# Optimization experiments

Hardware: AMD Instinct MI355X
Metric: run time of the kernel (lower is better)

The kernel has to match this reference:

```python
import jax, jax.numpy as jnp
import numpy as np
import math

N, L, C, H, K = 4, 16384, 256, 8, 4
D = C // H


def setup_inputs():
    rng = jax.random.key(0)
    ks = jax.random.split(rng, 16)
    def w(k, shape, scale):
        return jax.random.normal(k, shape, jnp.float32) * scale
    s = 1.0 / math.sqrt(C)
    return {
        "query": jax.random.normal(ks[0], (N, L, C), jnp.float32),
        "key": jax.random.normal(ks[1], (N, L, C), jnp.float32),
        "value": jax.random.normal(ks[2], (N, L, C), jnp.float32),
        "reference_points": jax.random.uniform(ks[3], (N, L, 2), jnp.float32),
        "pos_embed": jax.random.normal(ks[4], (N, L, C), jnp.float32),
        "Wq": w(ks[5], (C, C), s), "bq": jnp.zeros((C,), jnp.float32),
        "Wk": w(ks[6], (C, C), s), "bk": jnp.zeros((C,), jnp.float32),
        "Wv": w(ks[7], (C, C), s), "bv": jnp.zeros((C,), jnp.float32),
        "Wo1": w(ks[8], (C, 2 * C), s), "bo1": jnp.zeros((2 * C,), jnp.float32),
        "Wo2": w(ks[9], (2 * C, H * K * 2), 0.02), "bo2": w(ks[10], (H * K * 2,), 0.02),
        "Wpos": w(ks[11], (C, C), s), "bpos": jnp.zeros((C,), jnp.float32),
        "Wout": w(ks[12], (C, C), s), "bout": jnp.zeros((C,), jnp.float32),
    }


def _sample_weight(points):
    # F.grid_sample on a 1x1 feature map (bilinear, zeros padding, align_corners=False)
    # degenerates to a scalar weight: grid g = 2p-1, unnormalized c = g/2 = p - 0.5,
    # pixel-0 bilinear weight per axis = max(0, 1 - |c|).
    c = points - 0.5
    return jax.nn.relu(1.0 - jnp.abs(c[..., 0])) * jax.nn.relu(1.0 - jnp.abs(c[..., 1]))


def reference(query, key, value, reference_points, pos_embed,
              Wq, bq, Wk, bk, Wv, bv, Wo1, bo1, Wo2, bo2, Wpos, bpos, Wout, bout):
    Nb, Ln, Cd = query.shape
    q = (query @ Wq + bq).reshape(Nb, Ln, H, D)
    k = (key @ Wk + bk).reshape(Nb, Ln, H, D)
    v = (value @ Wv + bv).reshape(Nb, Ln, H, D)
    pos = (pos_embed @ Wpos + bpos).reshape(Nb, Ln, H, D)
    q = q + pos
    k = k + pos
    # offset MLP: Linear(C,2C) -> ReLU -> Linear(2C, H*K*2)
    offsets = (jax.nn.relu(query @ Wo1 + bo1) @ Wo2 + bo2).reshape(Nb, Ln, H, K, 2)
    sp = reference_points[:, :, None, None, :] + offsets  # [N,L,H,K,2]
    w = _sample_weight(sp)                                # [N,L,H,K]
    # sampled_k[n,l,h,k,:] = k[n,l,h,:] * w[n,l,h,k]  (1x1 grid_sample closed form)
    qk = jnp.einsum('nlhd,nlhd->nlh', q, k)               # [N,L,H]
    attn = jax.nn.softmax(qk[..., None] * w / math.sqrt(D), axis=-1)  # [N,L,H,K]
    # output = sum_k attn_k * (v * w_k) = v * sum_k(attn_k * w_k)
    wv = jnp.sum(attn * w, axis=-1)                       # [N,L,H]
    out = (v * wv[..., None]).reshape(Nb, Ln, Cd)
    return out @ Wout + bout
```

## Files before the change

kernel.cpp:

```cpp
#include <hip/hip_runtime.h>
#include <hip/hip_bf16.h>

typedef __bf16 bf16x8 __attribute__((ext_vector_type(8)));
typedef float f32x4 __attribute__((ext_vector_type(4)));
typedef float f32x2 __attribute__((ext_vector_type(2)));

#define MT 32
#define CC 256

__device__ __forceinline__ int swz(int r, int c) {
    return r * 512 + ((c * 2) ^ ((r & 7) << 4));
}

template<int MREP, int NREP, int NKS>
__device__ __forceinline__ void mfma_tile(const __bf16* A_lds, const __bf16* __restrict__ WT,
                                          int KC, int ct, int kt0,
                                          f32x4 (&acc)[MREP][NREP], int r16, int q4, int laneoff)
{
#pragma unroll
    for (int ks = 0; ks < NKS; ++ks) {
        int ak = ks * 32 + q4 * 8;
        bf16x8 a[MREP], b[NREP];
#pragma unroll
        for (int mf = 0; mf < MREP; ++mf)
            a[mf] = *(const bf16x8*)((const char*)A_lds + swz(mf * 16 + r16, ak));
#pragma unroll
        for (int nf = 0; nf < NREP; ++nf)
            b[nf] = *(const bf16x8*)(WT + ((size_t)(ct + nf) * KC + kt0 + ks) * 512 + laneoff);
#pragma unroll
        for (int mf = 0; mf < MREP; ++mf)
#pragma unroll
            for (int nf = 0; nf < NREP; ++nf)
                acc[mf][nf] = __builtin_amdgcn_mfma_f32_16x16x32_bf16(a[mf], b[nf], acc[mf][nf], 0, 0, 0);
    }
}

__device__ __forceinline__ void zero4(f32x4 (&acc)[2][4]) {
#pragma unroll
    for (int i = 0; i < 2; ++i)
#pragma unroll
        for (int j = 0; j < 4; ++j)
            acc[i][j] = (f32x4){0.f, 0.f, 0.f, 0.f};
}

__device__ __forceinline__ void stage_load(const float* __restrict__ src, int row0, int tid,
                                           f32x4 (&v)[8]) {
#pragma unroll
    for (int i = 0; i < 8; ++i) {
        int f = i * 256 + tid;
        int r = f >> 6;
        int c = (f & 63) * 4;
        v[i] = __builtin_nontemporal_load((const f32x4*)(src + (size_t)(row0 + r) * CC + c));
    }
}
__device__ __forceinline__ void stage_write(__bf16* dst, int tid, const f32x4 (&v)[8]) {
#pragma unroll
    for (int i = 0; i < 8; ++i) {
        int f = i * 256 + tid;
        int r = f >> 6;
        int c = (f & 63) * 4;
        union { __bf16 h[4]; unsigned long long u; } uu;
        uu.h[0] = (__bf16)v[i][0]; uu.h[1] = (__bf16)v[i][1];
        uu.h[2] = (__bf16)v[i][2]; uu.h[3] = (__bf16)v[i][3];
        *(unsigned long long*)((char*)dst + swz(r, c)) = uu.u;
    }
}

__global__ void prep_all(const float* __restrict__ Wq, const float* __restrict__ Wk,
                         const float* __restrict__ Wpos, const float* __restrict__ Wo1,
                         const float* __restrict__ Wo2, const float* __restrict__ Wv,
                         const float* __restrict__ Wout, __bf16* __restrict__ ws)
{
    int i = blockIdx.x * 256 + threadIdx.x;
    if (i >= 557056) return;
    int j, K, N;
    const float* S0 = nullptr; const float* S1 = nullptr;
    if (i < 131072)      { j = i;          K = 512; N = 256; S0 = Wq;  S1 = Wpos; }
    else if (i < 262144) { j = i - 131072; K = 512; N = 256; S0 = Wk;  S1 = Wpos; }
    else if (i < 393216) { j = i - 262144; K = 256; N = 512; S0 = Wo1; }
    else if (i < 425984) { j = i - 393216; K = 512; N = 64;  S0 = Wo2; }
    else if (i < 491520) { j = i - 425984; K = 256; N = 256; S0 = Wv; }
    else                 { j = i - 491520; K = 256; N = 256; S0 = Wout; }
    int tile = j >> 9, r = j & 511;
    int lane = r >> 3, e = r & 7;
    int q4 = lane >> 4, r16 = lane & 15;
    int KC = K >> 5;
    int nc = tile / KC, kc = tile - nc * KC;
    int k = kc * 32 + q4 * 8 + e;
    int n = nc * 16 + r16;
    float v;
    if (S1 && k >= 256) v = S1[(size_t)(k - 256) * N + n];
    else                v = S0[(size_t)k * N + n];
    ws[i] = (__bf16)v;
}

extern "C" __global__ void __launch_bounds__(256, 2)
k1_attn_weights(const float* __restrict__ query, const float* __restrict__ key,
                const float* __restrict__ pose, const float* __restrict__ refp,
                const __bf16* __restrict__ ws,
                const float* __restrict__ bq, const float* __restrict__ bk,
                const float* __restrict__ bpos, const float* __restrict__ bo1,
                const float* __restrict__ bo2,
                float* __restrict__ wv_g)
{
    const __bf16* WTqp = ws;
    const __bf16* WTkp = ws + 131072;
    const __bf16* WTo1 = ws + 262144;
    const __bf16* WTo2 = ws + 393216;

    __shared__ __attribute__((aligned(16))) __bf16 SA[MT * CC];
    __shared__ __attribute__((aligned(16))) __bf16 SB[MT * CC];
    __shared__ __attribute__((aligned(16))) __bf16 SC[MT * CC];
    __shared__ __attribute__((aligned(16))) __bf16 SD[MT * CC];
    __shared__ float off_s[MT * 64];

    const int tid = threadIdx.x;
    const int lane = tid & 63;
    const int wid = tid >> 6;
    const int r16 = lane & 15;
    const int q4 = lane >> 4;
    const int laneoff = lane * 8;
    const int row0 = blockIdx.x * MT;
    const int cb = wid * 64;
    const int ct = wid * 4;

    f32x4 acc[2][4];
    f32x4 accO[2];

    {
        f32x4 vq[8], vp[8];
        stage_load(query, row0, tid, vq);
        stage_load(pose, row0, tid, vp);
        stage_write(SA, tid, vq);
        stage_write(SB, tid, vp);
    }
    __syncthreads();

    f32x4 vkey[8];
    stage_load(key, row0, tid, vkey);
    zero4(acc);
    mfma_tile<2, 4, 8>(SA, WTo1, 8, ct, 0, acc, r16, q4, laneoff);
#pragma unroll
    for (int mf = 0; mf < 2; ++mf)
#pragma unroll
        for (int nf = 0; nf < 4; ++nf) {
            int col = cb + nf * 16 + r16;
            float bias = bo1[col];
#pragma unroll
            for (int r = 0; r < 4; ++r)
                *(__bf16*)((char*)SD + swz(mf * 16 + q4 * 4 + r, col)) =
                    (__bf16)fmaxf(acc[mf][nf][r] + bias, 0.f);
        }
    __syncthreads();

    accO[0] = (f32x4){0.f, 0.f, 0.f, 0.f};
    accO[1] = (f32x4){0.f, 0.f, 0.f, 0.f};
    {
        f32x4 (&aO)[2][1] = *(f32x4(*)[2][1])&accO;
        mfma_tile<2, 1, 8>(SD, WTo2, 16, wid, 0, aO, r16, q4, laneoff);
    }
    __syncthreads();

    stage_write(SC, tid, vkey);
    zero4(acc);
    mfma_tile<2, 4, 8>(SA, WTo1, 8, 16 + ct, 0, acc, r16, q4, laneoff);
#pragma unroll
    for (int mf = 0; mf < 2; ++mf)
#pragma unroll
        for (int nf = 0; nf < 4; ++nf) {
            int col = cb + nf * 16 + r16;
            float bias = bo1[256 + col];
#pragma unroll
            for (int r = 0; r < 4; ++r)
                *(__bf16*)((char*)SD + swz(mf * 16 + q4 * 4 + r, col)) =
                    (__bf16)fmaxf(acc[mf][nf][r] + bias, 0.f);
        }
    __syncthreads();

    {
        f32x4 (&aO)[2][1] = *(f32x4(*)[2][1])&accO;
        mfma_tile<2, 1, 8>(SD, WTo2, 16, wid, 8, aO, r16, q4, laneoff);
    }
    {
        int col = wid * 16 + r16;
        float b2 = bo2[col];
#pragma unroll
        for (int mf = 0; mf < 2; ++mf)
#pragma unroll
            for (int r = 0; r < 4; ++r)
                off_s[(mf * 16 + q4 * 4 + r) * 64 + col] = accO[mf][r] + b2;
    }
    __syncthreads();

    zero4(acc);
    mfma_tile<2, 4, 8>(SA, WTqp, 16, ct, 0, acc, r16, q4, laneoff);
    mfma_tile<2, 4, 8>(SB, WTqp, 16, ct, 8, acc, r16, q4, laneoff);
#pragma unroll
    for (int mf = 0; mf < 2; ++mf)
#pragma unroll
        for (int nf = 0; nf < 4; ++nf) {
            int col = cb + nf * 16 + r16;
            float bias = bq[col] + bpos[col];
#pragma unroll
            for (int r = 0; r < 4; ++r)
                *(__bf16*)((char*)SD + swz(mf * 16 + q4 * 4 + r, col)) =
                    (__bf16)(acc[mf][nf][r] + bias);
        }
    __syncthreads();

    zero4(acc);
    mfma_tile<2, 4, 8>(SC, WTkp, 16, ct, 0, acc, r16, q4, laneoff);
    mfma_tile<2, 4, 8>(SB, WTkp, 16, ct, 8, acc, r16, q4, laneoff);
#pragma unroll
    for (int mf = 0; mf < 2; ++mf)
#pragma unroll
        for (int nf = 0; nf < 4; ++nf) {
            int col = cb + nf * 16 + r16;
            float bias = bk[col] + bpos[col];
#pragma unroll
            for (int r = 0; r < 4; ++r)
                *(__bf16*)((char*)SA + swz(mf * 16 + q4 * 4 + r, col)) =
                    (__bf16)(acc[mf][nf][r] + bias);
        }
    __syncthreads();

    {
        int t = tid >> 3, h = tid & 7;
        float qk = 0.f;
#pragma unroll
        for (int j = 0; j < 4; ++j) {
            int c = h * 32 + j * 8;
            bf16x8 qv = *(const bf16x8*)((const char*)SD + swz(t, c));
            bf16x8 kv = *(const bf16x8*)((const char*)SA + swz(t, c));
#pragma unroll
            for (int e = 0; e < 8; ++e) qk += (float)qv[e] * (float)kv[e];
        }
        f32x2 rp = __builtin_nontemporal_load((const f32x2*)(refp + (size_t)(row0 + t) * 2));
        float wgt[4], lg[4];
        float m = -1e30f;
#pragma unroll
        for (int kk = 0; kk < 4; ++kk) {
            float2 o = *(const float2*)&off_s[t * 64 + (h * 4 + kk) * 2];
            float cx = rp[0] + o.x - 0.5f, cy = rp[1] + o.y - 0.5f;
            float wx = fmaxf(0.f, 1.f - fabsf(cx));
            float wy = fmaxf(0.f, 1.f - fabsf(cy));
            wgt[kk] = wx * wy;
            lg[kk] = qk * wgt[kk] * 0.17677669529663687f;
            m = fmaxf(m, lg[kk]);
        }
        float s = 0.f, sw = 0.f;
#pragma unroll
        for (int kk = 0; kk < 4; ++kk) {
            float e = __expf(lg[kk] - m);
            s += e;
            sw += e * wgt[kk];
        }
        __builtin_nontemporal_store(sw / s, wv_g + (size_t)(row0 + t) * 8 + h);
    }
}

extern "C" __global__ void __launch_bounds__(256, 4)
k2_output(const float* __restrict__ value, const float* __restrict__ wv_g,
          const __bf16* __restrict__ ws,
          const float* __restrict__ bv, const float* __restrict__ bout,
          float* __restrict__ out)
{
    const __bf16* WTv   = ws + 425984;
    const __bf16* WTout = ws + 491520;

    __shared__ __attribute__((aligned(16))) __bf16 SC[MT * 256];
    __shared__ __attribute__((aligned(16))) __bf16 SD[MT * 256];
    __shared__ float wv_s[MT * 8];

    const int tid = threadIdx.x;
    const int lane = tid & 63;
    const int wid = tid >> 6;
    const int r16 = lane & 15;
    const int q4 = lane >> 4;
    const int laneoff = lane * 8;
    const int row0 = blockIdx.x * MT;
    const int cb = wid * 64;
    const int ct = wid * 4;

    f32x4 acc[2][4];

    {
        f32x4 vv[8];
        stage_load(value, row0, tid, vv);
        wv_s[tid] = wv_g[(size_t)row0 * 8 + tid];
        stage_write(SC, tid, vv);
    }
    __syncthreads();

    zero4(acc);
    mfma_tile<2, 4, 8>(SC, WTv, 8, ct, 0, acc, r16, q4, laneoff);
#pragma unroll
    for (int mf = 0; mf < 2; ++mf)
#pragma unroll
        for (int nf = 0; nf < 4; ++nf) {
            int col = cb + nf * 16 + r16;
            float bias = bv[col];
#pragma unroll
            for (int r = 0; r < 4; ++r) {
                int row = mf * 16 + q4 * 4 + r;
                float wvv = wv_s[row * 8 + (col >> 5)];
                *(__bf16*)((char*)SD + swz(row, col)) = (__bf16)((acc[mf][nf][r] + bias) * wvv);
            }
        }
    __syncthreads();

    zero4(acc);
    mfma_tile<2, 4, 8>(SD, WTout, 8, ct, 0, acc, r16, q4, laneoff);
#pragma unroll
    for (int mf = 0; mf < 2; ++mf)
#pragma unroll
        for (int nf = 0; nf < 4; ++nf) {
            int col = cb + nf * 16 + r16;
            float bias = bout[col];
#pragma unroll
            for (int r = 0; r < 4; ++r) {
                int row = mf * 16 + q4 * 4 + r;
                __builtin_nontemporal_store(acc[mf][nf][r] + bias,
                                            out + (size_t)(row0 + row) * CC + col);
            }
        }
}

extern "C" void kernel_launch(void* const* d_in, const int* in_sizes, int n_in,
                              void* d_out, int out_size, void* d_ws, size_t ws_size,
                              hipStream_t stream)
{
    const float* query = (const float*)d_in[0];
    const float* key   = (const float*)d_in[1];
    const float* value = (const float*)d_in[2];
    const float* refp  = (const float*)d_in[3];
    const float* pose  = (const float*)d_in[4];
    const float* Wq  = (const float*)d_in[5];  const float* bq   = (const float*)d_in[6];
    const float* Wk  = (const float*)d_in[7];  const float* bk   = (const float*)d_in[8];
    const float* Wv  = (const float*)d_in[9];  const float* bv   = (const float*)d_in[10];
    const float* Wo1 = (const float*)d_in[11]; const float* bo1  = (const float*)d_in[12];
    const float* Wo2 = (const float*)d_in[13]; const float* bo2  = (const float*)d_in[14];
    const float* Wpos= (const float*)d_in[15]; const float* bpos = (const float*)d_in[16];
    const float* Wout= (const float*)d_in[17]; const float* bout = (const float*)d_in[18];

    __bf16* ws = (__bf16*)d_ws;
    float* wv_g = (float*)((char*)d_ws + 1114112);

    prep_all<<<2176, 256, 0, stream>>>(Wq, Wk, Wpos, Wo1, Wo2, Wv, Wout, ws);

    k1_attn_weights<<<65536 / MT, 256, 0, stream>>>(
        query, key, pose, refp, ws, bq, bk, bpos, bo1, bo2, wv_g);

    k2_output<<<65536 / MT, 256, 0, stream>>>(
        value, wv_g, ws, bv, bout, (float*)d_out);
}
```

Before: 164.2 us.

## Fuse attention-weight and output kernels into one per-tile kernel

Merges the two per-row-tile kernels into a single kernel, so the per-row head weights stay in shared memory and no longer go through a global buffer, and one launch is removed. The offset MLP's first layer now runs in one wide pass into a larger shared buffer instead of two halves. The Q and K projections are computed together and their dot product is reduced in registers with lane shuffles rather than written to LDS as bf16 and re-read. The cost is higher register pressure (16 accumulator tiles at once, plus the value tile prefetched early), which may reduce occupancy below the two blocks per CU requested.

```diff
diff --git a/kernel.cpp b/kernel.cpp
--- a/kernel.cpp
+++ b/kernel.cpp
@@ -11,28 +11,8 @@
 __device__ __forceinline__ int swz(int r, int c) {
     return r * 512 + ((c * 2) ^ ((r & 7) << 4));
 }
-
-template<int MREP, int NREP, int NKS>
-__device__ __forceinline__ void mfma_tile(const __bf16* A_lds, const __bf16* __restrict__ WT,
-                                          int KC, int ct, int kt0,
-                                          f32x4 (&acc)[MREP][NREP], int r16, int q4, int laneoff)
-{
-#pragma unroll
-    for (int ks = 0; ks < NKS; ++ks) {
-        int ak = ks * 32 + q4 * 8;
-        bf16x8 a[MREP], b[NREP];
-#pragma unroll
-        for (int mf = 0; mf < MREP; ++mf)
-            a[mf] = *(const bf16x8*)((const char*)A_lds + swz(mf * 16 + r16, ak));
-#pragma unroll
-        for (int nf = 0; nf < NREP; ++nf)
-            b[nf] = *(const bf16x8*)(WT + ((size_t)(ct + nf) * KC + kt0 + ks) * 512 + laneoff);
-#pragma unroll
-        for (int mf = 0; mf < MREP; ++mf)
-#pragma unroll
-            for (int nf = 0; nf < NREP; ++nf)
-                acc[mf][nf] = __builtin_amdgcn_mfma_f32_16x16x32_bf16(a[mf], b[nf], acc[mf][nf], 0, 0, 0);
-    }
+__device__ __forceinline__ int swzH(int r, int c) {
+    return r * 1024 + ((c * 2) ^ ((r & 7) << 4));
 }
 
 __device__ __forceinline__ void zero4(f32x4 (&acc)[2][4]) {
@@ -95,24 +75,31 @@
 }
 
 extern "C" __global__ void __launch_bounds__(256, 2)
-k1_attn_weights(const float* __restrict__ query, const float* __restrict__ key,
-                const float* __restrict__ pose, const float* __restrict__ refp,
-                const __bf16* __restrict__ ws,
-                const float* __restrict__ bq, const float* __restrict__ bk,
-                const float* __restrict__ bpos, const float* __restrict__ bo1,
-                const float* __restrict__ bo2,
-                float* __restrict__ wv_g)
+fused_ext_attn(const float* __restrict__ query, const float* __restrict__ key,
+               const float* __restrict__ value, const float* __restrict__ refp,
+               const float* __restrict__ pose,
+               const __bf16* __restrict__ ws,
+               const float* __restrict__ bq, const float* __restrict__ bk,
+               const float* __restrict__ bv, const float* __restrict__ bpos,
+               const float* __restrict__ bo1, const float* __restrict__ bo2,
+               const float* __restrict__ bout,
+               float* __restrict__ out)
 {
-    const __bf16* WTqp = ws;
-    const __bf16* WTkp = ws + 131072;
-    const __bf16* WTo1 = ws + 262144;
-    const __bf16* WTo2 = ws + 393216;
+    const __bf16* WTqp  = ws;
+    const __bf16* WTkp  = ws + 131072;
+    const __bf16* WTo1  = ws + 262144;
+    const __bf16* WTo2  = ws + 393216;
+    const __bf16* WTv   = ws + 425984;
+    const __bf16* WTout = ws + 491520;
 
     __shared__ __attribute__((aligned(16))) __bf16 SA[MT * CC];
     __shared__ __attribute__((aligned(16))) __bf16 SB[MT * CC];
     __shared__ __attribute__((aligned(16))) __bf16 SC[MT * CC];
-    __shared__ __attribute__((aligned(16))) __bf16 SD[MT * CC];
-    __shared__ float off_s[MT * 64];
+    __shared__ __attribute__((aligned(16))) char   H1[32768];
+
+    float* off_s = (float*)H1;
+    float* qk_s  = (float*)(H1 + 8192);
+    float* wv_s  = (float*)(H1 + 9216);
 
     const int tid = threadIdx.x;
     const int lane = tid & 63;
@@ -121,66 +108,67 @@
     const int q4 = lane >> 4;
     const int laneoff = lane * 8;
     const int row0 = blockIdx.x * MT;
-    const int cb = wid * 64;
-    const int ct = wid * 4;
-
-    f32x4 acc[2][4];
+
+    f32x4 vq[8], vp[8], vkey[8];
+    stage_load(query, row0, tid, vq);
+    stage_load(pose, row0, tid, vp);
+    stage_load(key, row0, tid, vkey);
+    stage_write(SA, tid, vq);
+    stage_write(SB, tid, vp);
+    __syncthreads();
+
+    stage_write(SC, tid, vkey);
+    {
+        f32x4 acc[2][8];
+#pragma unroll
+        for (int i = 0; i < 2; ++i)
+#pragma unroll
+            for (int j = 0; j < 8; ++j) acc[i][j] = (f32x4){0.f, 0.f, 0.f, 0.f};
+#pragma unroll
+        for (int ks = 0; ks < 8; ++ks) {
+            int ak = ks * 32 + q4 * 8;
+            bf16x8 a[2], b[8];
+#pragma unroll
+            for (int mf = 0; mf < 2; ++mf)
+                a[mf] = *(const bf16x8*)((const char*)SA + swz(mf * 16 + r16, ak));
+#pragma unroll
+            for (int nf = 0; nf < 8; ++nf)
+                b[nf] = *(const bf16x8*)(WTo1 + ((size_t)(wid * 8 + nf) * 8 + ks) * 512 + laneoff);
+#pragma unroll
+            for (int mf = 0; mf < 2; ++mf)
+#pragma unroll
+                for (int nf = 0; nf < 8; ++nf)
+                    acc[mf][nf] = __builtin_amdgcn_mfma_f32_16x16x32_bf16(a[mf], b[nf], acc[mf][nf], 0, 0, 0);
+        }
+#pragma unroll
+        for (int mf = 0; mf < 2; ++mf)
+#pragma unroll
+            for (int nf = 0; nf < 8; ++nf) {
+                int col = wid * 128 + nf * 16 + r16;
+                float bias = bo1[col];
+#pragma unroll
+                for (int r = 0; r < 4; ++r)
+                    *(__bf16*)(H1 + swzH(mf * 16 + q4 * 4 + r, col)) =
+                        (__bf16)fmaxf(acc[mf][nf][r] + bias, 0.f);
+            }
+    }
+    __syncthreads();
+
     f32x4 accO[2];
-
-    {
-        f32x4 vq[8], vp[8];
-        stage_load(query, row0, tid, vq);
-        stage_load(pose, row0, tid, vp);
-        stage_write(SA, tid, vq);
-        stage_write(SB, tid, vp);
-    }
-    __syncthreads();
-
-    f32x4 vkey[8];
-    stage_load(key, row0, tid, vkey);
-    zero4(acc);
-    mfma_tile<2, 4, 8>(SA, WTo1, 8, ct, 0, acc, r16, q4, laneoff);
-#pragma unroll
-    for (int mf = 0; mf < 2; ++mf)
-#pragma unroll
-        for (int nf = 0; nf < 4; ++nf) {
-            int col = cb + nf * 16 + r16;
-            float bias = bo1[col];
-#pragma unroll
-            for (int r = 0; r < 4; ++r)
-                *(__bf16*)((char*)SD + swz(mf * 16 + q4 * 4 + r, col)) =
-                    (__bf16)fmaxf(acc[mf][nf][r] + bias, 0.f);
-        }
-    __syncthreads();
-
     accO[0] = (f32x4){0.f, 0.f, 0.f, 0.f};
     accO[1] = (f32x4){0.f, 0.f, 0.f, 0.f};
-    {
-        f32x4 (&aO)[2][1] = *(f32x4(*)[2][1])&accO;
-        mfma_tile<2, 1, 8>(SD, WTo2, 16, wid, 0, aO, r16, q4, laneoff);
-    }
-    __syncthreads();
-
-    stage_write(SC, tid, vkey);
-    zero4(acc);
-    mfma_tile<2, 4, 8>(SA, WTo1, 8, 16 + ct, 0, acc, r16, q4, laneoff);
-#pragma unroll
-    for (int mf = 0; mf < 2; ++mf)
-#pragma unroll
-        for (int nf = 0; nf < 4; ++nf) {
-            int col = cb + nf * 16 + r16;
-            float bias = bo1[256 + col];
-#pragma unroll
-            for (int r = 0; r < 4; ++r)
-                *(__bf16*)((char*)SD + swz(mf * 16 + q4 * 4 + r, col)) =
-                    (__bf16)fmaxf(acc[mf][nf][r] + bias, 0.f);
-        }
-    __syncthreads();
-
-    {
-        f32x4 (&aO)[2][1] = *(f32x4(*)[2][1])&accO;
-        mfma_tile<2, 1, 8>(SD, WTo2, 16, wid, 8, aO, r16, q4, laneoff);
-    }
+#pragma unroll
+    for (int ks = 0; ks < 16; ++ks) {
+        int ak = ks * 32 + q4 * 8;
+        bf16x8 b = *(const bf16x8*)(WTo2 + ((size_t)wid * 16 + ks) * 512 + laneoff);
+#pragma unroll
+        for (int mf = 0; mf < 2; ++mf) {
+            bf16x8 a = *(const bf16x8*)(H1 + swzH(mf * 16 + r16, ak));
+            accO[mf] = __builtin_amdgcn_mfma_f32_16x16x32_bf16(a, b, accO[mf], 0, 0, 0);
+        }
+    }
+    __syncthreads();
+
     {
         int col = wid * 16 + r16;
         float b2 = bo2[col];
@@ -190,58 +178,91 @@
             for (int r = 0; r < 4; ++r)
                 off_s[(mf * 16 + q4 * 4 + r) * 64 + col] = accO[mf][r] + b2;
     }
-    __syncthreads();
-
-    zero4(acc);
-    mfma_tile<2, 4, 8>(SA, WTqp, 16, ct, 0, acc, r16, q4, laneoff);
-    mfma_tile<2, 4, 8>(SB, WTqp, 16, ct, 8, acc, r16, q4, laneoff);
-#pragma unroll
-    for (int mf = 0; mf < 2; ++mf)
+    f32x4 vval[8];
+    stage_load(value, row0, tid, vval);
+    {
+        f32x4 qa[2][4], ka[2][4];
+        zero4(qa); zero4(ka);
+#pragma unroll
+        for (int ks = 0; ks < 8; ++ks) {
+            int ak = ks * 32 + q4 * 8;
+            bf16x8 aq[2], akk[2];
+#pragma unroll
+            for (int mf = 0; mf < 2; ++mf) {
+                aq[mf]  = *(const bf16x8*)((const char*)SA + swz(mf * 16 + r16, ak));
+                akk[mf] = *(const bf16x8*)((const char*)SC + swz(mf * 16 + r16, ak));
+            }
+#pragma unroll
+            for (int nf = 0; nf < 4; ++nf) {
+                size_t toff = ((size_t)(wid * 4 + nf) * 16 + ks) * 512 + laneoff;
+                bf16x8 bqf = *(const bf16x8*)(WTqp + toff);
+                bf16x8 bkf = *(const bf16x8*)(WTkp + toff);
+#pragma unroll
+                for (int mf = 0; mf < 2; ++mf) {
+                    qa[mf][nf] = __builtin_amdgcn_mfma_f32_16x16x32_bf16(aq[mf],  bqf, qa[mf][nf], 0, 0, 0);
+                    ka[mf][nf] = __builtin_amdgcn_mfma_f32_16x16x32_bf16(akk[mf], bkf, ka[mf][nf], 0, 0, 0);
+                }
+            }
+        }
+#pragma unroll
+        for (int ks = 8; ks < 16; ++ks) {
+            int ak = (ks - 8) * 32 + q4 * 8;
+            bf16x8 ap[2];
+#pragma unroll
+            for (int mf = 0; mf < 2; ++mf)
+                ap[mf] = *(const bf16x8*)((const char*)SB + swz(mf * 16 + r16, ak));
+#pragma unroll
+            for (int nf = 0; nf < 4; ++nf) {
+                size_t toff = ((size_t)(wid * 4 + nf) * 16 + ks) * 512 + laneoff;
+                bf16x8 bqf = *(const bf16x8*)(WTqp + toff);
+                bf16x8 bkf = *(const bf16x8*)(WTkp + toff);
+#pragma unroll
+                for (int mf = 0; mf < 2; ++mf) {
+                    qa[mf][nf] = __builtin_amdgcn_mfma_f32_16x16x32_bf16(ap[mf], bqf, qa[mf][nf], 0, 0, 0);
+                    ka[mf][nf] = __builtin_amdgcn_mfma_f32_16x16x32_bf16(ap[mf], bkf, ka[mf][nf], 0, 0, 0);
+                }
+            }
+        }
+        float Bq[4], Bk[4];
 #pragma unroll
         for (int nf = 0; nf < 4; ++nf) {
-            int col = cb + nf * 16 + r16;
-            float bias = bq[col] + bpos[col];
-#pragma unroll
-            for (int r = 0; r < 4; ++r)
-                *(__bf16*)((char*)SD + swz(mf * 16 + q4 * 4 + r, col)) =
-                    (__bf16)(acc[mf][nf][r] + bias);
-        }
-    __syncthreads();
-
-    zero4(acc);
-    mfma_tile<2, 4, 8>(SC, WTkp, 16, ct, 0, acc, r16, q4, laneoff);
-    mfma_tile<2, 4, 8>(SB, WTkp, 16, ct, 8, acc, r16, q4, laneoff);
-#pragma unroll
-    for (int mf = 0; mf < 2; ++mf)
-#pragma unroll
-        for (int nf = 0; nf < 4; ++nf) {
-            int col = cb + nf * 16 + r16;
-            float bias = bk[col] + bpos[col];
-#pragma unroll
-            for (int r = 0; r < 4; ++r)
-                *(__bf16*)((char*)SA + swz(mf * 16 + q4 * 4 + r, col)) =
-                    (__bf16)(acc[mf][nf][r] + bias);
-        }
-    __syncthreads();
-
-    {
-        int t = tid >> 3, h = tid & 7;
-        float qk = 0.f;
-#pragma unroll
-        for (int j = 0; j < 4; ++j) {
-            int c = h * 32 + j * 8;
-            bf16x8 qv = *(const bf16x8*)((const char*)SD + swz(t, c));
-            bf16x8 kv = *(const bf16x8*)((const char*)SA + swz(t, c));
-#pragma unroll
-            for (int e = 0; e < 8; ++e) qk += (float)qv[e] * (float)kv[e];
-        }
+            int col = wid * 64 + nf * 16 + r16;
+            Bq[nf] = bq[col] + bpos[col];
+            Bk[nf] = bk[col] + bpos[col];
+        }
+#pragma unroll
+        for (int mf = 0; mf < 2; ++mf)
+#pragma unroll
+            for (int r = 0; r < 4; ++r) {
+                float p0 = (qa[mf][0][r] + Bq[0]) * (ka[mf][0][r] + Bk[0])
+                         + (qa[mf][1][r] + Bq[1]) * (ka[mf][1][r] + Bk[1]);
+                float p1 = (qa[mf][2][r] + Bq[2]) * (ka[mf][2][r] + Bk[2])
+                         + (qa[mf][3][r] + Bq[3]) * (ka[mf][3][r] + Bk[3]);
+#pragma unroll
+                for (int m = 1; m < 16; m <<= 1) {
+                    p0 += __shfl_xor(p0, m);
+                    p1 += __shfl_xor(p1, m);
+                }
+                if (r16 == 0) {
+                    int row = mf * 16 + q4 * 4 + r;
+                    f32x2 pq = {p0, p1};
+                    *(f32x2*)&qk_s[row * 8 + wid * 2] = pq;
+                }
+            }
+    }
+    asm volatile("s_waitcnt lgkmcnt(0)" ::: "memory");
+    __builtin_amdgcn_sched_barrier(0);
+    {
+        int t = lane >> 1, h = wid * 2 + (lane & 1);
+        float qk = qk_s[t * 8 + h];
         f32x2 rp = __builtin_nontemporal_load((const f32x2*)(refp + (size_t)(row0 + t) * 2));
         float wgt[4], lg[4];
         float m = -1e30f;
 #pragma unroll
         for (int kk = 0; kk < 4; ++kk) {
-            float2 o = *(const float2*)&off_s[t * 64 + (h * 4 + kk) * 2];
-            float cx = rp[0] + o.x - 0.5f, cy = rp[1] + o.y - 0.5f;
+            float ox = off_s[t * 64 + (h * 4 + kk) * 2];
+            float oy = off_s[t * 64 + (h * 4 + kk) * 2 + 1];
+            float cx = rp[0] + ox - 0.5f, cy = rp[1] + oy - 0.5f;
             float wx = fmaxf(0.f, 1.f - fabsf(cx));
             float wy = fmaxf(0.f, 1.f - fabsf(cy));
             wgt[kk] = wx * wy;
@@ -255,75 +276,81 @@
             s += e;
             sw += e * wgt[kk];
         }
-        __builtin_nontemporal_store(sw / s, wv_g + (size_t)(row0 + t) * 8 + h);
-    }
-}
-
-extern "C" __global__ void __launch_bounds__(256, 4)
-k2_output(const float* __restrict__ value, const float* __restrict__ wv_g,
-          const __bf16* __restrict__ ws,
-          const float* __restrict__ bv, const float* __restrict__ bout,
-          float* __restrict__ out)
-{
-    const __bf16* WTv   = ws + 425984;
-    const __bf16* WTout = ws + 491520;
-
-    __shared__ __attribute__((aligned(16))) __bf16 SC[MT * 256];
-    __shared__ __attribute__((aligned(16))) __bf16 SD[MT * 256];
-    __shared__ float wv_s[MT * 8];
-
-    const int tid = threadIdx.x;
-    const int lane = tid & 63;
-    const int wid = tid >> 6;
-    const int r16 = lane & 15;
-    const int q4 = lane >> 4;
-    const int laneoff = lane * 8;
-    const int row0 = blockIdx.x * MT;
-    const int cb = wid * 64;
-    const int ct = wid * 4;
-
-    f32x4 acc[2][4];
-
-    {
-        f32x4 vv[8];
-        stage_load(value, row0, tid, vv);
-        wv_s[tid] = wv_g[(size_t)row0 * 8 + tid];
-        stage_write(SC, tid, vv);
-    }
-    __syncthreads();
-
-    zero4(acc);
-    mfma_tile<2, 4, 8>(SC, WTv, 8, ct, 0, acc, r16, q4, laneoff);
-#pragma unroll
-    for (int mf = 0; mf < 2; ++mf)
-#pragma unroll
-        for (int nf = 0; nf < 4; ++nf) {
-            int col = cb + nf * 16 + r16;
-            float bias = bv[col];
-#pragma unroll
-            for (int r = 0; r < 4; ++r) {
-                int row = mf * 16 + q4 * 4 + r;
-                float wvv = wv_s[row * 8 + (col >> 5)];
-                *(__bf16*)((char*)SD + swz(row, col)) = (__bf16)((acc[mf][nf][r] + bias) * wvv);
-            }
-        }
-    __syncthreads();
-
-    zero4(acc);
-    mfma_tile<2, 4, 8>(SD, WTout, 8, ct, 0, acc, r16, q4, laneoff);
-#pragma unroll
-    for (int mf = 0; mf < 2; ++mf)
-#pragma unroll
-        for (int nf = 0; nf < 4; ++nf) {
-            int col = cb + nf * 16 + r16;
-            float bias = bout[col];
-#pragma unroll
-            for (int r = 0; r < 4; ++r) {
-                int row = mf * 16 + q4 * 4 + r;
-                __builtin_nontemporal_store(acc[mf][nf][r] + bias,
-                                            out + (size_t)(row0 + row) * CC + col);
-            }
-        }
+        wv_s[t * 8 + h] = sw / s;
+    }
+    __syncthreads();
+
+    stage_write(SA, tid, vval);
+    __syncthreads();
+
+    {
+        f32x4 acc[2][4];
+        zero4(acc);
+#pragma unroll
+        for (int ks = 0; ks < 8; ++ks) {
+            int ak = ks * 32 + q4 * 8;
+            bf16x8 a[2], b[4];
+#pragma unroll
+            for (int mf = 0; mf < 2; ++mf)
+                a[mf] = *(const bf16x8*)((const char*)SA + swz(mf * 16 + r16, ak));
+#pragma unroll
+            for (int nf = 0; nf < 4; ++nf)
+                b[nf] = *(const bf16x8*)(WTv + ((size_t)(wid * 4 + nf) * 8 + ks) * 512 + laneoff);
+#pragma unroll
+            for (int mf = 0; mf < 2; ++mf)
+#pragma unroll
+                for (int nf = 0; nf < 4; ++nf)
+                    acc[mf][nf] = __builtin_amdgcn_mfma_f32_16x16x32_bf16(a[mf], b[nf], acc[mf][nf], 0, 0, 0);
+        }
+#pragma unroll
+        for (int mf = 0; mf < 2; ++mf)
+#pragma unroll
+            for (int nf = 0; nf < 4; ++nf) {
+                int col = wid * 64 + nf * 16 + r16;
+                float bias = bv[col];
+#pragma unroll
+                for (int r = 0; r < 4; ++r) {
+                    int row = mf * 16 + q4 * 4 + r;
+                    float wvv = wv_s[row * 8 + (col >> 5)];
+                    *(__bf16*)((char*)SC + swz(row, col)) = (__bf16)((acc[mf][nf][r] + bias) * wvv);
+                }
+            }
+    }
+    __syncthreads();
+
+    {
+        f32x4 acc[2][4];
+        zero4(acc);
+#pragma unroll
+        for (int ks = 0; ks < 8; ++ks) {
+            int ak = ks * 32 + q4 * 8;
+            bf16x8 a[2], b[4];
+#pragma unroll
+            for (int mf = 0; mf < 2; ++mf)
+                a[mf] = *(const bf16x8*)((const char*)SC + swz(mf * 16 + r16, ak));
+#pragma unroll
+            for (int nf = 0; nf < 4; ++nf)
+                b[nf] = *(const bf16x8*)(WTout + ((size_t)(wid * 4 + nf) * 8 + ks) * 512 + laneoff);
+#pragma unroll
+            for (int mf = 0; mf < 2; ++mf)
+#pragma unroll
+                for (int nf = 0; nf < 4; ++nf)
+                    acc[mf][nf] = __builtin_amdgcn_mfma_f32_16x16x32_bf16(a[mf], b[nf], acc[mf][nf], 0, 0, 0);
+        }
+#pragma unroll
+        for (int mf = 0; mf < 2; ++mf)
+#pragma unroll
+            for (int nf = 0; nf < 4; ++nf) {
+                int col = wid * 64 + nf * 16 + r16;
+                float bias = bout[col];
+#pragma unroll
+                for (int r = 0; r < 4; ++r) {
+                    int row = mf * 16 + q4 * 4 + r;
+                    __builtin_nontemporal_store(acc[mf][nf][r] + bias,
+                                                out + (size_t)(row0 + row) * CC + col);
+                }
+            }
+    }
 }
 
 extern "C" void kernel_launch(void* const* d_in, const int* in_sizes, int n_in,
@@ -344,13 +371,10 @@
     const float* Wout= (const float*)d_in[17]; const float* bout = (const float*)d_in[18];
 
     __bf16* ws = (__bf16*)d_ws;
-    float* wv_g = (float*)((char*)d_ws + 1114112);
 
     prep_all<<<2176, 256, 0, stream>>>(Wq, Wk, Wpos, Wo1, Wo2, Wv, Wout, ws);
 
-    k1_attn_weights<<<65536 / MT, 256, 0, stream>>>(
-        query, key, pose, refp, ws, bq, bk, bpos, bo1, bo2, wv_g);
-
-    k2_output<<<65536 / MT, 256, 0, stream>>>(
-        value, wv_g, ws, bv, bout, (float*)d_out);
-}
+    fused_ext_attn<<<65536 / MT, 256, 0, stream>>>(
+        query, key, value, refp, pose, ws,
+        bq, bk, bv, bpos, bo1, bo2, bout, (float*)d_out);
+}
```

After: 150.5 us. 8.3% less time.
